# Performance work log

Hardware: AMD Instinct MI355X
Metric: run time of the kernel (lower is better)

The kernel has to match this reference:

```python
import jax, jax.numpy as jnp
import numpy as np

B = 65536
LAYERS = [256, 512, 512, 256]


def setup_inputs() -> dict:
    key = jax.random.key(0)
    ks = jax.random.split(key, 10)
    inp = {"data": jax.random.normal(ks[0], (B, LAYERS[0]), dtype=jnp.float32)}
    for i in range(3):
        n_in, n_out = LAYERS[i], LAYERS[i + 1]
        # link weights ~ U[0,1) like random.random(); bias params[0] zeroed in torch code
        inp[f"W{i+1}"] = jax.random.uniform(ks[1 + 3 * i], (n_in, n_out), dtype=jnp.float32)
        inp[f"b{i+1}"] = jnp.zeros((n_out,), dtype=jnp.float32)
        # per-node activation params a = params[1:6], torch.rand init
        inp[f"a{i+1}"] = jax.random.uniform(ks[2 + 3 * i], (n_out, 5), dtype=jnp.float32)
    return inp


def _act(x, a):
    # x: [B, n], a: [n, 5]; a0*tanh(x)*sin(a1*x+a2) + a3*x + a4  (per-node params broadcast over batch)
    return a[:, 0] * jnp.tanh(x) * jnp.sin(a[:, 1] * x + a[:, 2]) + a[:, 3] * x + a[:, 4]


def reference(data, W1, b1, a1, W2, b2, a2, W3, b3, a3):
    h = _act(data @ W1 + b1, a1)
    h = _act(h @ W2 + b2, a2)
    h = _act(h @ W3 + b3, a3)
    return jax.nn.softmax(h, axis=1)
```

## Files before the change

### kernel.cpp

```cpp
#include <hip/hip_runtime.h>

#define BATCH 65536

typedef float f32x4 __attribute__((ext_vector_type(4)));
typedef _Float16 f16x8 __attribute__((ext_vector_type(8)));

__device__ __forceinline__ void async_ld16(const void* g, void* l) {
  __builtin_amdgcn_global_load_lds(
      (const __attribute__((address_space(1))) void*)g,
      (__attribute__((address_space(3))) void*)l, 16, 0, 0);
}

__device__ __forceinline__ float act_f(float x, float a0, float a1, float a2,
                                       float a3, float a4) {
  float ax = fabsf(x);
  float e = __builtin_amdgcn_exp2f(ax * -2.8853900817779268f);
  float th = (1.0f - e) * __builtin_amdgcn_rcpf(1.0f + e);
  th = copysignf(th, x);
  float arg = fmaf(a1, x, a2);
  float rev = arg * 0.15915494309189535f;
  rev -= floorf(rev);
  float s = __builtin_amdgcn_sinf(rev);
  return fmaf(a3, x, fmaf(a0 * th, s, a4));
}

__global__ __launch_bounds__(256) void splitT_k(const float* __restrict__ W,
                                                _Float16* __restrict__ hi,
                                                _Float16* __restrict__ lo,
                                                int K, int N) {
  const int i = blockIdx.x * 256 + threadIdx.x;
  if (i >= K * N) return;
  const int k = i / N, n = i % N;
  const float w = W[i];
  const _Float16 h = (_Float16)w;
  hi[(size_t)n * K + k] = h;
  lo[(size_t)n * K + k] = (_Float16)(w - (float)h);
}

__global__ __launch_bounds__(256) void prep_params(const float* __restrict__ b,
                                                   const float* __restrict__ a,
                                                   float* __restrict__ Pt,
                                                   int N) {
  const int c = blockIdx.x * 256 + threadIdx.x;
  if (c >= N) return;
  Pt[c] = b[c];
#pragma unroll
  for (int j = 0; j < 5; ++j) Pt[(1 + j) * N + c] = a[c * 5 + j];
}

__device__ __forceinline__ f32x4 mfma3s(f16x8 wh, f16x8 wl, f16x8 xh,
                                        f16x8 xl, f32x4 c) {
  c = __builtin_amdgcn_mfma_f32_16x16x32_f16(wh, xh, c, 0, 0, 0);
  c = __builtin_amdgcn_mfma_f32_16x16x32_f16(wh, xl, c, 0, 0, 0);
  c = __builtin_amdgcn_mfma_f32_16x16x32_f16(wl, xh, c, 0, 0, 0);
  return c;
}

template <bool AF32, bool FINAL, int NW>
__global__ __launch_bounds__(256, NW) void gemm_act(
    const float* __restrict__ Af, const _Float16* __restrict__ Ahi,
    const _Float16* __restrict__ Alo, const _Float16* __restrict__ Bhi,
    const _Float16* __restrict__ Blo, const float* __restrict__ Pt,
    _Float16* __restrict__ Chi, _Float16* __restrict__ Clo,
    float* __restrict__ Cout, int K, int N) {
  __shared__ __align__(16) _Float16 smem[20480];
  _Float16* sA = smem;
  _Float16* sB = smem + 4096;

  const int tid = threadIdx.x;
  const int wv = tid >> 6, lane = tid & 63;
  const int m16 = lane & 15, quad = lane >> 4;
  const int col0 = blockIdx.x * 256;
  const int row0 = blockIdx.y * 64;
  const int rl4 = lane >> 2, sg4 = (lane & 3) ^ ((rl4 >> 1) & 3);
  const int rl8 = lane >> 3, sg8 = (lane & 7) ^ rl8;
  const int fswz = (quad ^ ((m16 >> 1) & 3)) * 8;
  const int rc7 = m16 & 7;

  f32x4 acc[4][4];
  const f32x4 zero = {0.f, 0.f, 0.f, 0.f};
#pragma unroll
  for (int i = 0; i < 4; ++i)
#pragma unroll
    for (int j = 0; j < 4; ++j) acc[i][j] = zero;

  const int nk = K >> 5;
  for (int kt = 0; kt < nk; ++kt) {
    const int k0 = kt << 5;
    if constexpr (AF32) {
      float* sAf = (float*)sA;
#pragma unroll
      for (int t = 0; t < 2; ++t) {
        const int c = wv * 2 + t;
        const size_t ga = (size_t)(row0 + c * 8 + rl8) * K + k0 + sg8 * 4;
        async_ld16(Af + ga, (void*)&sAf[c * 256]);
      }
    } else {
      const int c = wv;
      const size_t ga = (size_t)(row0 + c * 16 + rl4) * K + k0 + sg4 * 8;
      async_ld16(Ahi + ga, (void*)&sA[c * 512]);
      async_ld16(Alo + ga, (void*)&sA[2048 + c * 512]);
    }
#pragma unroll
    for (int t = 0; t < 4; ++t) {
      const int c = wv * 4 + t;
      const size_t gb = (size_t)(col0 + c * 16 + rl4) * K + k0 + sg4 * 8;
      async_ld16(Bhi + gb, (void*)&sB[c * 512]);
      async_ld16(Blo + gb, (void*)&sB[8192 + c * 512]);
    }
    __syncthreads();

    f16x8 ah[4], al[4];
#pragma unroll
    for (int tm = 0; tm < 4; ++tm) {
      const int arow = tm * 16 + m16;
      if constexpr (AF32) {
        const float* sAf = (const float*)sA + arow * 32;
        const f32x4 x0 = *(const f32x4*)(sAf + ((2 * quad) ^ rc7) * 4);
        const f32x4 x1 = *(const f32x4*)(sAf + ((2 * quad + 1) ^ rc7) * 4);
#pragma unroll
        for (int j = 0; j < 4; ++j) {
          const _Float16 h0 = (_Float16)x0[j];
          ah[tm][j] = h0;
          al[tm][j] = (_Float16)(x0[j] - (float)h0);
          const _Float16 h1 = (_Float16)x1[j];
          ah[tm][4 + j] = h1;
          al[tm][4 + j] = (_Float16)(x1[j] - (float)h1);
        }
      } else {
        const int idx = arow * 32 + fswz;
        ah[tm] = *(const f16x8*)&sA[idx];
        al[tm] = *(const f16x8*)&sA[2048 + idx];
      }
    }
#pragma unroll
    for (int tn = 0; tn < 4; ++tn) {
      const int bcol = wv * 64 + tn * 16 + m16;
      const int idx = bcol * 32 + fswz;
      const f16x8 bh = *(const f16x8*)&sB[idx];
      const f16x8 bl = *(const f16x8*)&sB[8192 + idx];
#pragma unroll
      for (int tm = 0; tm < 4; ++tm)
        acc[tm][tn] = mfma3s(bh, bl, ah[tm], al[tm], acc[tm][tn]);
    }
    __syncthreads();
  }

  if constexpr (!FINAL) {
    float* ly = (float*)smem;
#pragma unroll
    for (int p = 0; p < 2; ++p) {
#pragma unroll
      for (int j = 0; j < 2; ++j) {
        const int tn = 2 * p + j;
        const int colb = col0 + wv * 64 + tn * 16 + quad * 4;
        f32x4 P[6];
#pragma unroll
        for (int q = 0; q < 6; ++q) P[q] = *(const f32x4*)&Pt[q * N + colb];
#pragma unroll
        for (int tm = 0; tm < 4; ++tm) {
          const int row = tm * 16 + m16;
          f32x4 y;
#pragma unroll
          for (int r = 0; r < 4; ++r)
            y[r] = act_f(acc[tm][tn][r] + P[0][r], P[1][r], P[2][r], P[3][r],
                         P[4][r], P[5][r]);
          const int g = (wv * 8 + j * 4 + quad) ^ (row & 7);
          *(f32x4*)&ly[row * 128 + g * 4] = y;
        }
      }
      __syncthreads();
#pragma unroll
      for (int i = 0; i < 4; ++i) {
        const int u = tid + 256 * i;
        const int row = u >> 4, oct = u & 15;
        const int g0 = (2 * oct) ^ (row & 7), g1 = (2 * oct + 1) ^ (row & 7);
        const f32x4 a = *(const f32x4*)&ly[row * 128 + g0 * 4];
        const f32x4 b = *(const f32x4*)&ly[row * 128 + g1 * 4];
        f16x8 h8, l8;
#pragma unroll
        for (int r = 0; r < 4; ++r) {
          const _Float16 ha = (_Float16)a[r];
          h8[r] = ha;
          l8[r] = (_Float16)(a[r] - (float)ha);
          const _Float16 hb = (_Float16)b[r];
          h8[4 + r] = hb;
          l8[4 + r] = (_Float16)(b[r] - (float)hb);
        }
        const int gcol = (oct >> 2) * 64 + p * 32 + (oct & 3) * 8;
        const size_t o = (size_t)(row0 + row) * N + col0 + gcol;
        *(f16x8*)&Chi[o] = h8;
        *(f16x8*)&Clo[o] = l8;
      }
      __syncthreads();
    }
  } else {
    const float L2E = 1.4426950408889634f;
    float mx[4], sm[4];
#pragma unroll
    for (int tm = 0; tm < 4; ++tm) mx[tm] = -1e30f;
#pragma unroll
    for (int tn = 0; tn < 4; ++tn) {
      const int colb = wv * 64 + tn * 16 + quad * 4;
      f32x4 P[6];
#pragma unroll
      for (int q = 0; q < 6; ++q) P[q] = *(const f32x4*)&Pt[q * 256 + colb];
#pragma unroll
      for (int tm = 0; tm < 4; ++tm)
#pragma unroll
        for (int r = 0; r < 4; ++r) {
          const float y = act_f(acc[tm][tn][r] + P[0][r], P[1][r], P[2][r],
                                P[3][r], P[4][r], P[5][r]);
          acc[tm][tn][r] = y;
          mx[tm] = fmaxf(mx[tm], y);
        }
    }
#pragma unroll
    for (int tm = 0; tm < 4; ++tm) {
      mx[tm] = fmaxf(mx[tm], __shfl_xor(mx[tm], 16));
      mx[tm] = fmaxf(mx[tm], __shfl_xor(mx[tm], 32));
    }
    float* part = (float*)smem;
    if (quad == 0) {
#pragma unroll
      for (int tm = 0; tm < 4; ++tm) part[wv * 64 + tm * 16 + m16] = mx[tm];
    }
    __syncthreads();
#pragma unroll
    for (int tm = 0; tm < 4; ++tm) {
      const int rl = tm * 16 + m16;
      float M = part[rl];
#pragma unroll
      for (int w = 1; w < 4; ++w) M = fmaxf(M, part[w * 64 + rl]);
      mx[tm] = M;
      sm[tm] = 0.f;
    }
#pragma unroll
    for (int tn = 0; tn < 4; ++tn)
#pragma unroll
      for (int tm = 0; tm < 4; ++tm)
#pragma unroll
        for (int r = 0; r < 4; ++r) {
          const float e =
              __builtin_amdgcn_exp2f((acc[tm][tn][r] - mx[tm]) * L2E);
          acc[tm][tn][r] = e;
          sm[tm] += e;
        }
#pragma unroll
    for (int tm = 0; tm < 4; ++tm) {
      sm[tm] += __shfl_xor(sm[tm], 16);
      sm[tm] += __shfl_xor(sm[tm], 32);
    }
    __syncthreads();
    if (quad == 0) {
#pragma unroll
      for (int tm = 0; tm < 4; ++tm)
        part[256 + wv * 64 + tm * 16 + m16] = sm[tm];
    }
    __syncthreads();
    float sc[4];
#pragma unroll
    for (int tm = 0; tm < 4; ++tm) {
      const int rl = tm * 16 + m16;
      float S = part[256 + rl];
#pragma unroll
      for (int w = 1; w < 4; ++w) S += part[256 + w * 64 + rl];
      sc[tm] = __builtin_amdgcn_rcpf(S);
    }
#pragma unroll
    for (int tn = 0; tn < 4; ++tn) {
      const int colb = wv * 64 + tn * 16 + quad * 4;
#pragma unroll
      for (int tm = 0; tm < 4; ++tm) {
        const int row = row0 + tm * 16 + m16;
        f32x4 v = acc[tm][tn];
#pragma unroll
        for (int r = 0; r < 4; ++r) v[r] *= sc[tm];
        *(f32x4*)&Cout[(size_t)row * 256 + colb] = v;
      }
    }
  }
}

extern "C" void kernel_launch(void* const* d_in, const int* in_sizes, int n_in,
                              void* d_out, int out_size, void* d_ws,
                              size_t ws_size, hipStream_t stream) {
  const float* data = (const float*)d_in[0];
  const float* W1 = (const float*)d_in[1];
  const float* b1 = (const float*)d_in[2];
  const float* a1 = (const float*)d_in[3];
  const float* W2 = (const float*)d_in[4];
  const float* b2 = (const float*)d_in[5];
  const float* a2 = (const float*)d_in[6];
  const float* W3 = (const float*)d_in[7];
  const float* b3 = (const float*)d_in[8];
  const float* a3 = (const float*)d_in[9];
  float* out = (float*)d_out;

  char* ws = (char*)d_ws;
  const size_t KB = 1024;
  _Float16* w1hi = (_Float16*)(ws + 0 * KB);
  _Float16* w1lo = (_Float16*)(ws + 256 * KB);
  _Float16* w2hi = (_Float16*)(ws + 512 * KB);
  _Float16* w2lo = (_Float16*)(ws + 1024 * KB);
  _Float16* w3hi = (_Float16*)(ws + 1536 * KB);
  _Float16* w3lo = (_Float16*)(ws + 1792 * KB);
  float* Pt1 = (float*)(ws + 2048 * KB);
  float* Pt2 = (float*)(ws + 2064 * KB);
  float* Pt3 = (float*)(ws + 2080 * KB);
  _Float16* h1hi = (_Float16*)(ws + 2112 * KB);
  _Float16* h1lo = (_Float16*)(ws + 2112 * KB + (size_t)BATCH * 512 * 2);
  _Float16* h2lo = (_Float16*)(ws + 2112 * KB + (size_t)BATCH * 512 * 4);
  _Float16* h2hi = (_Float16*)d_out;

  splitT_k<<<(256 * 512 + 255) / 256, 256, 0, stream>>>(W1, w1hi, w1lo, 256, 512);
  splitT_k<<<(512 * 512 + 255) / 256, 256, 0, stream>>>(W2, w2hi, w2lo, 512, 512);
  splitT_k<<<(512 * 256 + 255) / 256, 256, 0, stream>>>(W3, w3hi, w3lo, 512, 256);
  prep_params<<<2, 256, 0, stream>>>(b1, a1, Pt1, 512);
  prep_params<<<2, 256, 0, stream>>>(b2, a2, Pt2, 512);
  prep_params<<<1, 256, 0, stream>>>(b3, a3, Pt3, 256);

  gemm_act<true, false, 4><<<dim3(2, BATCH / 64), 256, 0, stream>>>(
      data, nullptr, nullptr, w1hi, w1lo, Pt1, h1hi, h1lo, nullptr, 256, 512);
  gemm_act<false, false, 4><<<dim3(2, BATCH / 64), 256, 0, stream>>>(
      nullptr, h1hi, h1lo, w2hi, w2lo, Pt2, h2hi, h2lo, nullptr, 512, 512);
  gemm_act<false, true, 3><<<dim3(1, BATCH / 64), 256, 0, stream>>>(
      nullptr, h2hi, h2lo, w3hi, w3lo, Pt3, nullptr, nullptr, out, 512, 256);
}
```

Before: 472.6 us.

## Store intermediate activations as fp32 and split A into hi/lo at load time

Intermediate layer outputs are now written straight from registers to global memory as fp32, dropping the LDS-staged fp16 hi/lo split in the epilogue. Every layer then reads fp32 A and splits it into fp16 hi/lo when loading fragments. The layer-2 output is split into two 256-column halves, one in the output buffer and one in workspace, and layer 3 reads both through a dual-A path. Global traffic stays the same bytes (fp32 versus two fp16 arrays) and the epilogue shuffle and barriers are removed, but the epilogue stores are now less coalesced and the per-tile A conversion adds ALU work.

```diff
diff --git a/kernel.cpp b/kernel.cpp
--- a/kernel.cpp
+++ b/kernel.cpp
@@ -56,13 +56,12 @@
   return c;
 }
 
-template <bool AF32, bool FINAL, int NW>
+template <bool DUALA, bool SPLITC, bool FINAL, int NW>
 __global__ __launch_bounds__(256, NW) void gemm_act(
-    const float* __restrict__ Af, const _Float16* __restrict__ Ahi,
-    const _Float16* __restrict__ Alo, const _Float16* __restrict__ Bhi,
-    const _Float16* __restrict__ Blo, const float* __restrict__ Pt,
-    _Float16* __restrict__ Chi, _Float16* __restrict__ Clo,
-    float* __restrict__ Cout, int K, int N) {
+    const float* __restrict__ Af0, const float* __restrict__ Af1,
+    const _Float16* __restrict__ Bhi, const _Float16* __restrict__ Blo,
+    const float* __restrict__ Pt, float* __restrict__ C0,
+    float* __restrict__ C1, float* __restrict__ Cout, int K, int N) {
   __shared__ __align__(16) _Float16 smem[20480];
   _Float16* sA = smem;
   _Float16* sB = smem + 4096;
@@ -87,19 +86,25 @@
   const int nk = K >> 5;
   for (int kt = 0; kt < nk; ++kt) {
     const int k0 = kt << 5;
-    if constexpr (AF32) {
+    {
+      const float* Ab;
+      int koff, AK;
+      if constexpr (DUALA) {
+        Ab = (k0 < 256) ? Af0 : Af1;
+        koff = k0 & 255;
+        AK = 256;
+      } else {
+        Ab = Af0;
+        koff = k0;
+        AK = K;
+      }
       float* sAf = (float*)sA;
 #pragma unroll
       for (int t = 0; t < 2; ++t) {
         const int c = wv * 2 + t;
-        const size_t ga = (size_t)(row0 + c * 8 + rl8) * K + k0 + sg8 * 4;
-        async_ld16(Af + ga, (void*)&sAf[c * 256]);
-      }
-    } else {
-      const int c = wv;
-      const size_t ga = (size_t)(row0 + c * 16 + rl4) * K + k0 + sg4 * 8;
-      async_ld16(Ahi + ga, (void*)&sA[c * 512]);
-      async_ld16(Alo + ga, (void*)&sA[2048 + c * 512]);
+        const size_t ga = (size_t)(row0 + c * 8 + rl8) * AK + koff + sg8 * 4;
+        async_ld16(Ab + ga, (void*)&sAf[c * 256]);
+      }
     }
 #pragma unroll
     for (int t = 0; t < 4; ++t) {
@@ -114,23 +119,17 @@
 #pragma unroll
     for (int tm = 0; tm < 4; ++tm) {
       const int arow = tm * 16 + m16;
-      if constexpr (AF32) {
-        const float* sAf = (const float*)sA + arow * 32;
-        const f32x4 x0 = *(const f32x4*)(sAf + ((2 * quad) ^ rc7) * 4);
-        const f32x4 x1 = *(const f32x4*)(sAf + ((2 * quad + 1) ^ rc7) * 4);
-#pragma unroll
-        for (int j = 0; j < 4; ++j) {
-          const _Float16 h0 = (_Float16)x0[j];
-          ah[tm][j] = h0;
-          al[tm][j] = (_Float16)(x0[j] - (float)h0);
-          const _Float16 h1 = (_Float16)x1[j];
-          ah[tm][4 + j] = h1;
-          al[tm][4 + j] = (_Float16)(x1[j] - (float)h1);
-        }
-      } else {
-        const int idx = arow * 32 + fswz;
-        ah[tm] = *(const f16x8*)&sA[idx];
-        al[tm] = *(const f16x8*)&sA[2048 + idx];
+      const float* sAf = (const float*)sA + arow * 32;
+      const f32x4 x0 = *(const f32x4*)(sAf + ((2 * quad) ^ rc7) * 4);
+      const f32x4 x1 = *(const f32x4*)(sAf + ((2 * quad + 1) ^ rc7) * 4);
+#pragma unroll
+      for (int j = 0; j < 4; ++j) {
+        const _Float16 h0 = (_Float16)x0[j];
+        ah[tm][j] = h0;
+        al[tm][j] = (_Float16)(x0[j] - (float)h0);
+        const _Float16 h1 = (_Float16)x1[j];
+        ah[tm][4 + j] = h1;
+        al[tm][4 + j] = (_Float16)(x1[j] - (float)h1);
       }
     }
 #pragma unroll
@@ -147,52 +146,25 @@
   }
 
   if constexpr (!FINAL) {
-    float* ly = (float*)smem;
-#pragma unroll
-    for (int p = 0; p < 2; ++p) {
-#pragma unroll
-      for (int j = 0; j < 2; ++j) {
-        const int tn = 2 * p + j;
-        const int colb = col0 + wv * 64 + tn * 16 + quad * 4;
-        f32x4 P[6];
-#pragma unroll
-        for (int q = 0; q < 6; ++q) P[q] = *(const f32x4*)&Pt[q * N + colb];
-#pragma unroll
-        for (int tm = 0; tm < 4; ++tm) {
-          const int row = tm * 16 + m16;
-          f32x4 y;
-#pragma unroll
-          for (int r = 0; r < 4; ++r)
-            y[r] = act_f(acc[tm][tn][r] + P[0][r], P[1][r], P[2][r], P[3][r],
-                         P[4][r], P[5][r]);
-          const int g = (wv * 8 + j * 4 + quad) ^ (row & 7);
-          *(f32x4*)&ly[row * 128 + g * 4] = y;
-        }
-      }
-      __syncthreads();
-#pragma unroll
-      for (int i = 0; i < 4; ++i) {
-        const int u = tid + 256 * i;
-        const int row = u >> 4, oct = u & 15;
-        const int g0 = (2 * oct) ^ (row & 7), g1 = (2 * oct + 1) ^ (row & 7);
-        const f32x4 a = *(const f32x4*)&ly[row * 128 + g0 * 4];
-        const f32x4 b = *(const f32x4*)&ly[row * 128 + g1 * 4];
-        f16x8 h8, l8;
-#pragma unroll
-        for (int r = 0; r < 4; ++r) {
-          const _Float16 ha = (_Float16)a[r];
-          h8[r] = ha;
-          l8[r] = (_Float16)(a[r] - (float)ha);
-          const _Float16 hb = (_Float16)b[r];
-          h8[4 + r] = hb;
-          l8[4 + r] = (_Float16)(b[r] - (float)hb);
-        }
-        const int gcol = (oct >> 2) * 64 + p * 32 + (oct & 3) * 8;
-        const size_t o = (size_t)(row0 + row) * N + col0 + gcol;
-        *(f16x8*)&Chi[o] = h8;
-        *(f16x8*)&Clo[o] = l8;
-      }
-      __syncthreads();
+    float* Cb = SPLITC ? (blockIdx.x ? C1 : C0) : C0;
+    const int cstr = SPLITC ? 256 : N;
+#pragma unroll
+    for (int tn = 0; tn < 4; ++tn) {
+      const int cb = wv * 64 + tn * 16 + quad * 4;
+      const int gcol = col0 + cb;
+      f32x4 P[6];
+#pragma unroll
+      for (int q = 0; q < 6; ++q) P[q] = *(const f32x4*)&Pt[q * N + gcol];
+#pragma unroll
+      for (int tm = 0; tm < 4; ++tm) {
+        const int row = row0 + tm * 16 + m16;
+        f32x4 y;
+#pragma unroll
+        for (int r = 0; r < 4; ++r)
+          y[r] = act_f(acc[tm][tn][r] + P[0][r], P[1][r], P[2][r], P[3][r],
+                       P[4][r], P[5][r]);
+        *(f32x4*)&Cb[(size_t)row * cstr + (SPLITC ? cb : gcol)] = y;
+      }
     }
   } else {
     const float L2E = 1.4426950408889634f;
@@ -298,7 +270,7 @@
   float* out = (float*)d_out;
 
   char* ws = (char*)d_ws;
-  const size_t KB = 1024;
+  const size_t KB = 1024, MB = 1024 * 1024;
   _Float16* w1hi = (_Float16*)(ws + 0 * KB);
   _Float16* w1lo = (_Float16*)(ws + 256 * KB);
   _Float16* w2hi = (_Float16*)(ws + 512 * KB);
@@ -308,10 +280,9 @@
   float* Pt1 = (float*)(ws + 2048 * KB);
   float* Pt2 = (float*)(ws + 2064 * KB);
   float* Pt3 = (float*)(ws + 2080 * KB);
-  _Float16* h1hi = (_Float16*)(ws + 2112 * KB);
-  _Float16* h1lo = (_Float16*)(ws + 2112 * KB + (size_t)BATCH * 512 * 2);
-  _Float16* h2lo = (_Float16*)(ws + 2112 * KB + (size_t)BATCH * 512 * 4);
-  _Float16* h2hi = (_Float16*)d_out;
+  float* h1 = (float*)(ws + 4 * MB);
+  float* h2b = (float*)(ws + 4 * MB + 128 * MB);
+  float* h2a = (float*)d_out;
 
   splitT_k<<<(256 * 512 + 255) / 256, 256, 0, stream>>>(W1, w1hi, w1lo, 256, 512);
   splitT_k<<<(512 * 512 + 255) / 256, 256, 0, stream>>>(W2, w2hi, w2lo, 512, 512);
@@ -320,10 +291,10 @@
   prep_params<<<2, 256, 0, stream>>>(b2, a2, Pt2, 512);
   prep_params<<<1, 256, 0, stream>>>(b3, a3, Pt3, 256);
 
-  gemm_act<true, false, 4><<<dim3(2, BATCH / 64), 256, 0, stream>>>(
-      data, nullptr, nullptr, w1hi, w1lo, Pt1, h1hi, h1lo, nullptr, 256, 512);
-  gemm_act<false, false, 4><<<dim3(2, BATCH / 64), 256, 0, stream>>>(
-      nullptr, h1hi, h1lo, w2hi, w2lo, Pt2, h2hi, h2lo, nullptr, 512, 512);
-  gemm_act<false, true, 3><<<dim3(1, BATCH / 64), 256, 0, stream>>>(
-      nullptr, h2hi, h2lo, w3hi, w3lo, Pt3, nullptr, nullptr, out, 512, 256);
-}
+  gemm_act<false, false, false, 4><<<dim3(2, BATCH / 64), 256, 0, stream>>>(
+      data, nullptr, w1hi, w1lo, Pt1, h1, nullptr, nullptr, 256, 512);
+  gemm_act<false, true, false, 4><<<dim3(2, BATCH / 64), 256, 0, stream>>>(
+      h1, nullptr, w2hi, w2lo, Pt2, h2a, h2b, nullptr, 512, 512);
+  gemm_act<true, false, true, 3><<<dim3(1, BATCH / 64), 256, 0, stream>>>(
+      h2a, h2b, w3hi, w3lo, Pt3, nullptr, nullptr, out, 512, 256);
+}
```

Result: slower. 524.5 us (+11.0%).
